# Kernel tuning notes

Measured on AMD Instinct MI355X. Metric: run time of the kernel, lower is better.

## Reference

```python
import jax, jax.numpy as jnp
import numpy as np

CAP_FACTOR = 0.125  # capacity_factor from init_kwargs


def setup_inputs() -> dict:
    key = jax.random.key(0)
    k1, k2, k3, k4 = jax.random.split(key, 4)
    B, S, D, F = 4, 4096, 1024, 4096
    x = jax.random.normal(k1, (B, S, D), jnp.float32)
    w_router = jax.random.normal(k2, (D,), jnp.float32) * (D ** -0.5)
    W1 = jax.random.normal(k3, (D, F), jnp.float32) * (D ** -0.5)
    W2 = jax.random.normal(k4, (F, D), jnp.float32) * (F ** -0.5)
    return {"x": x, "w_router": w_router, "W1": W1, "W2": W2}


def reference(x, w_router, W1, W2):
    B, S, D = x.shape
    capacity = int(S * CAP_FACTOR)  # training-mode capacity (static)

    # router: Linear(dim,1,bias=False) + sigmoid -> [B, S]
    rw = jax.nn.sigmoid(jnp.einsum('bsd,d->bs', x, w_router))

    # topk over seq dim, then sort selected indices
    _, top_idx = jax.lax.top_k(rw, capacity)          # [B, cap]
    idx_sorted = jnp.sort(top_idx, axis=1)            # router_top_indices
    order = jnp.argsort(top_idx, axis=1)              # router_top_order (in [0, cap))

    # faithful to the original code: weights gathered from router_weights at
    # `order` positions (which index the first `capacity` sequence slots)
    w_top = jnp.take_along_axis(rw, order, axis=1)    # [B, cap]

    # gather selected tokens and run the submodule (gelu MLP)
    mod_x = jnp.take_along_axis(x, idx_sorted[:, :, None], axis=1)  # [B, cap, D]
    h = jax.nn.gelu(jnp.einsum('bcd,df->bcf', mod_x, W1))
    mod_out = jnp.einsum('bcf,fd->bcd', h, W2) * w_top[:, :, None]

    # scatter back to full sequence (indices are unique per batch)
    bidx = jnp.arange(B)[:, None]
    out = jnp.zeros_like(x).at[bidx, idx_sorted].set(mod_out)

    # BCE aux loss: targets are 1 at selected positions (log clamped at -100,
    # matching F.binary_cross_entropy)
    tgt = jnp.zeros_like(rw).at[bidx, idx_sorted].set(1.0)
    logw = jnp.maximum(jnp.log(rw), -100.0)
    log1mw = jnp.maximum(jnp.log1p(-rw), -100.0)
    mod_loss = -jnp.mean(tgt * logw + (1.0 - tgt) * log1mw)

    return out, mod_loss
```

## Files before the change

kernel.cpp:

```cpp
#include <hip/hip_runtime.h>
#include <stdint.h>

#define BB 4
#define SS 4096
#define DD 1024
#define FF 4096
#define CAP 512
#define MTOT (BB*CAP)
#define NOUT (BB*SS*DD)

typedef unsigned short ushort_t;
typedef float  float4v  __attribute__((ext_vector_type(4)));
typedef short  short8v  __attribute__((ext_vector_type(8)));
typedef unsigned short ushort4v __attribute__((ext_vector_type(4)));

#define OFF_RW   0u
#define OFF_IDX  (64u*1024u)
#define OFF_WTOP (72u*1024u)
#define OFF_LOSS (80u*1024u)
#define OFF_POS  (128u*1024u)
#define OFF_RANK (256u*1024u)
#define OFF_A    (1u<<20)
#define OFF_W1T  (5u<<20)
#define OFF_W2T  (13u<<20)
#define OFF_H    (21u<<20)
#define OFF_O    (37u<<20)

#define GLD16(gsrc, ldst) __builtin_amdgcn_global_load_lds( \
    (const __attribute__((address_space(1))) void*)(gsrc),  \
    (__attribute__((address_space(3))) void*)(ldst), 16, 0, 0)

__device__ inline ushort_t f2bf(float f) {
  uint32_t u = __builtin_bit_cast(uint32_t, f);
  u = u + 0x7fffu + ((u >> 16) & 1u);
  return (ushort_t)(u >> 16);
}

__global__ void router_kernel(const float* __restrict__ x, const float* __restrict__ w,
                              float* __restrict__ rw) {
  int wave = threadIdx.x >> 6;
  int lane = threadIdx.x & 63;
  int row  = blockIdx.x * 4 + wave;
  const float4* xr = (const float4*)(x + (size_t)row * DD);
  const float4* wr = (const float4*)w;
  float s = 0.f;
#pragma unroll
  for (int i = 0; i < 4; i++) {
    float4 a = xr[lane + i * 64];
    float4 b = wr[lane + i * 64];
    s += a.x * b.x + a.y * b.y + a.z * b.z + a.w * b.w;
  }
#pragma unroll
  for (int off = 32; off > 0; off >>= 1) s += __shfl_xor(s, off, 64);
  if (lane == 0) rw[row] = 1.f / (1.f + expf(-s));
}

__global__ __launch_bounds__(256) void rank_kernel(const float* __restrict__ rw,
                                                   int* __restrict__ rank) {
  __shared__ float v[SS];
  const int b = blockIdx.y;
  const float* rwg = rw + (size_t)b * SS;
  for (int m = threadIdx.x; m < SS / 4; m += 256)
    ((float4*)v)[m] = ((const float4*)rwg)[m];
  __syncthreads();
  const int e = blockIdx.x * 64 + (threadIdx.x >> 2);
  const int part = threadIdx.x & 3;
  const float vi = v[e];
  const int j0 = part * (SS / 4);
  int cnt = 0;
#pragma unroll 4
  for (int j4 = 0; j4 < SS / 16; ++j4) {
    float4 w = ((const float4*)(v + j0))[j4];
    int j = j0 + j4 * 4;
    cnt += (w.x > vi || (w.x == vi && (j + 0) < e));
    cnt += (w.y > vi || (w.y == vi && (j + 1) < e));
    cnt += (w.z > vi || (w.z == vi && (j + 2) < e));
    cnt += (w.w > vi || (w.w == vi && (j + 3) < e));
  }
  cnt += __shfl_xor(cnt, 1, 64);
  cnt += __shfl_xor(cnt, 2, 64);
  if (part == 0) rank[(size_t)b * SS + e] = cnt;
}

__global__ __launch_bounds__(1024) void finalize_kernel(const float* __restrict__ rw,
                                                        const int* __restrict__ rank,
                                                        int* __restrict__ idxs,
                                                        float* __restrict__ wtop,
                                                        int* __restrict__ posmap,
                                                        float* __restrict__ lossP) {
  __shared__ int   wsumI[16];
  __shared__ float wsumF[16];
  const int b = blockIdx.x, tid = threadIdx.x;
  const int lane = tid & 63, wv = tid >> 6;
  const float* rwg = rw + (size_t)b * SS;
  const int*   rkg = rank + (size_t)b * SS;
  const int m0 = tid * 4;
  int rk[4]; float rv[4];
  int cnt = 0;
#pragma unroll
  for (int u = 0; u < 4; u++) {
    rk[u] = rkg[m0 + u]; rv[u] = rwg[m0 + u];
    cnt += (rk[u] < CAP);
  }
  int val = cnt;
#pragma unroll
  for (int off = 1; off < 64; off <<= 1) {
    int n = __shfl_up(val, off, 64);
    if (lane >= off) val += n;
  }
  if (lane == 63) wsumI[wv] = val;
  __syncthreads();
  int wbase = 0;
  for (int w = 0; w < wv; ++w) wbase += wsumI[w];
  int excl = wbase + val - cnt;
#pragma unroll
  for (int u = 0; u < 4; u++) {
    int m = m0 + u;
    if (rk[u] < CAP) {
      int pos = excl++;
      idxs[b * CAP + pos] = m;
      wtop[b * CAP + pos] = rwg[rk[u]];
      posmap[(size_t)b * SS + m] = b * CAP + pos;
    } else {
      posmap[(size_t)b * SS + m] = -1;
    }
  }
  float ls = 0.f;
#pragma unroll
  for (int u = 0; u < 4; u++) {
    float term = (rk[u] < CAP) ? logf(rv[u]) : log1pf(-rv[u]);
    ls += fmaxf(term, -100.f);
  }
#pragma unroll
  for (int off = 32; off > 0; off >>= 1) ls += __shfl_xor(ls, off, 64);
  if (lane == 0) wsumF[wv] = ls;
  __syncthreads();
  if (tid == 0) {
    float t = 0.f;
    for (int i = 0; i < 16; i++) t += wsumF[i];
    lossP[b] = t;
  }
}

__global__ void transpose2_kernel(const float* __restrict__ W1, ushort_t* __restrict__ W1T,
                                  const float* __restrict__ W2, ushort_t* __restrict__ W2T) {
  __shared__ float t[32][33];
  int id = blockIdx.x;
  const float* in; ushort_t* out; int R, C, bx, by;
  if (id < (FF / 32) * (DD / 32)) {
    in = W1; out = W1T; R = DD; C = FF;
    bx = id % (FF / 32); by = id / (FF / 32);
  } else {
    id -= (FF / 32) * (DD / 32);
    in = W2; out = W2T; R = FF; C = DD;
    bx = id % (DD / 32); by = id / (DD / 32);
  }
  const int c0 = bx * 32, r0 = by * 32;
  const int tx = threadIdx.x;
  const int ty = threadIdx.y;
  const float4 vv = *(const float4*)&in[(size_t)(r0 + ty) * C + c0 + tx * 4];
  t[ty][tx * 4 + 0] = vv.x; t[ty][tx * 4 + 1] = vv.y;
  t[ty][tx * 4 + 2] = vv.z; t[ty][tx * 4 + 3] = vv.w;
  __syncthreads();
  ushort4v o;
  o[0] = f2bf(t[tx * 4 + 0][ty]); o[1] = f2bf(t[tx * 4 + 1][ty]);
  o[2] = f2bf(t[tx * 4 + 2][ty]); o[3] = f2bf(t[tx * 4 + 3][ty]);
  *(ushort4v*)&out[(size_t)(c0 + ty) * R + r0 + tx * 4] = o;
}

__global__ void gather_kernel(const float* __restrict__ x, const int* __restrict__ idxs,
                              ushort_t* __restrict__ A) {
  int row = blockIdx.x;
  int b = row >> 9;
  int seq = idxs[row];
  const float4* src = (const float4*)(x + ((size_t)(b * SS + seq)) * DD);
  float4 a = src[threadIdx.x];
  ushort4v o;
  o[0] = f2bf(a.x); o[1] = f2bf(a.y); o[2] = f2bf(a.z); o[3] = f2bf(a.w);
  *(ushort4v*)(A + (size_t)row * DD + threadIdx.x * 4) = o;
}

__global__ void scatter_kernel(const float* __restrict__ O, const int* __restrict__ posmap,
                               const float* __restrict__ wtop, const float* __restrict__ lossP,
                               float* __restrict__ out) {
  int r = blockIdx.x;
  int p = posmap[r];
  float4 v = {0.f, 0.f, 0.f, 0.f};
  if (p >= 0) {
    float wt = wtop[p];
    float4 v0 = ((const float4*)(O + (size_t)p * DD))[threadIdx.x];
    float4 v1 = ((const float4*)(O + (size_t)(MTOT * DD) + (size_t)p * DD))[threadIdx.x];
    v.x = (v0.x + v1.x) * wt; v.y = (v0.y + v1.y) * wt;
    v.z = (v0.z + v1.z) * wt; v.w = (v0.w + v1.w) * wt;
  }
  ((float4*)(out + (size_t)r * DD))[threadIdx.x] = v;
  if (r == 0 && threadIdx.x == 0)
    out[NOUT] = -(lossP[0] + lossP[1] + lossP[2] + lossP[3]) / (float)(BB * SS);
}

template <int MODE>
__global__ __launch_bounds__(256) void gemm_oc(const ushort_t* __restrict__ Ag,
                                               const ushort_t* __restrict__ Bg, int Kstride,
                                               ushort_t* __restrict__ Hout,
                                               float* __restrict__ Oacc) {
  __shared__ ushort_t lA[64 * 64];
  __shared__ ushort_t lB[64 * 64];
  const int tid = threadIdx.x;
  const int lane = tid & 63, wv = tid >> 6;
  const int wr = wv >> 1, wc = wv & 1;

  const int gx = gridDim.x, gy = gridDim.y;
  const int nwg = gx * gy * gridDim.z;
  int id = blockIdx.x + gx * (blockIdx.y + gy * blockIdx.z);
  int sw = (id & 7) * (nwg >> 3) + (id >> 3);
  const int bx = sw % gx;
  const int by = (sw / gx) % gy;
  const int bz = sw / (gx * gy);

  const int bm0 = by * 64, bn0 = bx * 64;
  const int kchunk = Kstride / gridDim.z;
  const int kbeg = bz * kchunk;
  const int nkt = kchunk / 64;

  const int srow = lane >> 3;
  const int gslot = (lane & 7) ^ srow;

  float4v acc[2][2];
#pragma unroll
  for (int i = 0; i < 2; i++)
#pragma unroll
    for (int j = 0; j < 2; j++) acc[i][j] = (float4v){0.f, 0.f, 0.f, 0.f};

  for (int t = 0; t < nkt; ++t) {
    const int k0 = kbeg + t * 64;
    __syncthreads();
#pragma unroll
    for (int i = 0; i < 2; i++) {
      const int chunkbase = i * 256 + wv * 64;
      const int row = i * 32 + wv * 8 + srow;
      const ushort_t* ga = Ag + (size_t)(bm0 + row) * Kstride + k0 + gslot * 8;
      GLD16(ga, &lA[chunkbase * 8]);
    }
#pragma unroll
    for (int i = 0; i < 2; i++) {
      const int chunkbase = i * 256 + wv * 64;
      const int row = i * 32 + wv * 8 + srow;
      const ushort_t* gb = Bg + (size_t)(bn0 + row) * Kstride + k0 + gslot * 8;
      GLD16(gb, &lB[chunkbase * 8]);
    }
    __syncthreads();
#pragma unroll
    for (int kk = 0; kk < 2; kk++) {
      const int s = (lane >> 4) + kk * 4;
      short8v af[2], bfr[2];
#pragma unroll
      for (int mi = 0; mi < 2; mi++) {
        const int rr = wr * 32 + mi * 16 + (lane & 15);
        af[mi] = *(const short8v*)&lA[rr * 64 + (s ^ (rr & 7)) * 8];
      }
#pragma unroll
      for (int nj = 0; nj < 2; nj++) {
        const int rr = wc * 32 + nj * 16 + (lane & 15);
        bfr[nj] = *(const short8v*)&lB[rr * 64 + (s ^ (rr & 7)) * 8];
      }
#pragma unroll
      for (int mi = 0; mi < 2; mi++)
#pragma unroll
        for (int nj = 0; nj < 2; nj++)
          acc[mi][nj] = __builtin_amdgcn_mfma_f32_16x16x32_bf16(af[mi], bfr[nj], acc[mi][nj], 0, 0, 0);
    }
  }

  if (MODE == 0) {
#pragma unroll
    for (int mi = 0; mi < 2; mi++) {
      int r0 = bm0 + wr * 32 + mi * 16 + ((lane >> 4) << 2);
#pragma unroll
      for (int nj = 0; nj < 2; nj++) {
        int cc = bn0 + wc * 32 + nj * 16 + (lane & 15);
#pragma unroll
        for (int r = 0; r < 4; r++) {
          float xv = acc[mi][nj][r];
          float g = 0.5f * xv * (1.f + tanhf(0.7978845608028654f * (xv + 0.044715f * xv * xv * xv)));
          Hout[(size_t)(r0 + r) * FF + cc] = f2bf(g);
        }
      }
    }
  } else {
    float* Op = Oacc + (size_t)bz * MTOT * DD;
#pragma unroll
    for (int mi = 0; mi < 2; mi++) {
      int tr0 = bm0 + wr * 32 + mi * 16 + ((lane >> 4) << 2);
#pragma unroll
      for (int r = 0; r < 4; r++) {
        float* orow = Op + (size_t)(tr0 + r) * DD + bn0 + wc * 32 + (lane & 15);
#pragma unroll
        for (int nj = 0; nj < 2; nj++) orow[nj * 16] = acc[mi][nj][r];
      }
    }
  }
}

extern "C" void kernel_launch(void* const* d_in, const int* in_sizes, int n_in,
                              void* d_out, int out_size, void* d_ws, size_t ws_size,
                              hipStream_t stream) {
  (void)in_sizes; (void)n_in; (void)out_size; (void)ws_size;
  const float* x  = (const float*)d_in[0];
  const float* wrt = (const float*)d_in[1];
  const float* W1 = (const float*)d_in[2];
  const float* W2 = (const float*)d_in[3];
  float* out = (float*)d_out;
  char* ws = (char*)d_ws;
  float*    rw   = (float*)(ws + OFF_RW);
  int*      idxs = (int*)(ws + OFF_IDX);
  float*    wtop = (float*)(ws + OFF_WTOP);
  float*    lossP= (float*)(ws + OFF_LOSS);
  int*      posm = (int*)(ws + OFF_POS);
  int*      rnk  = (int*)(ws + OFF_RANK);
  ushort_t* A    = (ushort_t*)(ws + OFF_A);
  ushort_t* W1T  = (ushort_t*)(ws + OFF_W1T);
  ushort_t* W2T  = (ushort_t*)(ws + OFF_W2T);
  ushort_t* H    = (ushort_t*)(ws + OFF_H);
  float*    O    = (float*)(ws + OFF_O);

  router_kernel<<<dim3(BB * SS / 4), dim3(256), 0, stream>>>(x, wrt, rw);
  rank_kernel<<<dim3(SS / 64, BB), dim3(256), 0, stream>>>(rw, rnk);
  finalize_kernel<<<dim3(BB), dim3(1024), 0, stream>>>(rw, rnk, idxs, wtop, posm, lossP);
  transpose2_kernel<<<dim3((FF / 32) * (DD / 32) * 2), dim3(8, 32), 0, stream>>>(W1, W1T, W2, W2T);
  gather_kernel<<<dim3(MTOT), dim3(256), 0, stream>>>(x, idxs, A);
  gemm_oc<0><<<dim3(FF / 64, MTOT / 64, 1), dim3(256), 0, stream>>>(A, W1T, DD, H, nullptr);
  gemm_oc<1><<<dim3(DD / 64, MTOT / 64, 2), dim3(256), 0, stream>>>(H, W2T, FF, nullptr, O);
  scatter_kernel<<<dim3(BB * SS), dim3(256), 0, stream>>>(O, posm, wtop, lossP, out);
}
```

Measured before the change: 136.0 us.

## Deepen GEMM K-step, use XCD-aware tile mapping, split-K 4 and faster GELU

The GEMM kernel now stages two 64-wide K slices per barrier pair, a 128-deep K step that halves the number of __syncthreads per tile. Block-to-tile mapping is now chosen explicitly per XCD so neighbouring tiles share A/B rows in the same L2. The second GEMM uses split-K of 4 instead of 2, and the scatter kernel sums four partial buffers. GELU's tanh is replaced by an equivalent exp-based sigmoid form. The trade-off is twice the shared memory per block, and the larger split-K adds partial-buffer traffic that could reduce occupancy or add memory pressure.

After: 130.0 us. -4.4%, faster.

```diff
diff --git a/kernel.cpp b/kernel.cpp
--- a/kernel.cpp
+++ b/kernel.cpp
@@ -188,10 +188,15 @@
   float4 v = {0.f, 0.f, 0.f, 0.f};
   if (p >= 0) {
     float wt = wtop[p];
+    const size_t stride = (size_t)MTOT * DD;
     float4 v0 = ((const float4*)(O + (size_t)p * DD))[threadIdx.x];
-    float4 v1 = ((const float4*)(O + (size_t)(MTOT * DD) + (size_t)p * DD))[threadIdx.x];
-    v.x = (v0.x + v1.x) * wt; v.y = (v0.y + v1.y) * wt;
-    v.z = (v0.z + v1.z) * wt; v.w = (v0.w + v1.w) * wt;
+    float4 v1 = ((const float4*)(O + stride + (size_t)p * DD))[threadIdx.x];
+    float4 v2 = ((const float4*)(O + 2 * stride + (size_t)p * DD))[threadIdx.x];
+    float4 v3 = ((const float4*)(O + 3 * stride + (size_t)p * DD))[threadIdx.x];
+    v.x = ((v0.x + v1.x) + (v2.x + v3.x)) * wt;
+    v.y = ((v0.y + v1.y) + (v2.y + v3.y)) * wt;
+    v.z = ((v0.z + v1.z) + (v2.z + v3.z)) * wt;
+    v.w = ((v0.w + v1.w) + (v2.w + v3.w)) * wt;
   }
   ((float4*)(out + (size_t)r * DD))[threadIdx.x] = v;
   if (r == 0 && threadIdx.x == 0)
@@ -203,24 +208,29 @@
                                                const ushort_t* __restrict__ Bg, int Kstride,
                                                ushort_t* __restrict__ Hout,
                                                float* __restrict__ Oacc) {
-  __shared__ ushort_t lA[64 * 64];
-  __shared__ ushort_t lB[64 * 64];
+  __shared__ ushort_t lA[2][64 * 64];
+  __shared__ ushort_t lB[2][64 * 64];
   const int tid = threadIdx.x;
   const int lane = tid & 63, wv = tid >> 6;
   const int wr = wv >> 1, wc = wv & 1;
 
   const int gx = gridDim.x, gy = gridDim.y;
-  const int nwg = gx * gy * gridDim.z;
-  int id = blockIdx.x + gx * (blockIdx.y + gy * blockIdx.z);
-  int sw = (id & 7) * (nwg >> 3) + (id >> 3);
-  const int bx = sw % gx;
-  const int by = (sw / gx) % gy;
-  const int bz = sw / (gx * gy);
-
-  const int bm0 = by * 64, bn0 = bx * 64;
-  const int kchunk = Kstride / gridDim.z;
-  const int kbeg = bz * kchunk;
-  const int nkt = kchunk / 64;
+  const int id = blockIdx.x + gx * (blockIdx.y + gy * blockIdx.z);
+  const int xcd = id & 7, q = id >> 3;
+
+  int bm0, bn0, bz, kbeg;
+  if (MODE == 0) {
+    const int mx = (xcd & 1) * 16 + (q & 15);
+    const int nx = (xcd >> 1) * 16 + (q >> 4);
+    bm0 = mx * 64; bn0 = nx * 64; bz = 0; kbeg = 0;
+  } else {
+    bz = xcd >> 1;
+    const int by = (xcd & 1) * 16 + (q & 15);
+    const int bx = q >> 4;
+    bm0 = by * 64; bn0 = bx * 64; kbeg = bz * (Kstride >> 2);
+  }
+  const int kchunk = (MODE == 0) ? Kstride : (Kstride >> 2);
+  const int nkt = kchunk / 128;
 
   const int srow = lane >> 3;
   const int gslot = (lane & 7) ^ srow;
@@ -232,36 +242,33 @@
     for (int j = 0; j < 2; j++) acc[i][j] = (float4v){0.f, 0.f, 0.f, 0.f};
 
   for (int t = 0; t < nkt; ++t) {
-    const int k0 = kbeg + t * 64;
+    const int k0 = kbeg + t * 128;
     __syncthreads();
 #pragma unroll
-    for (int i = 0; i < 2; i++) {
-      const int chunkbase = i * 256 + wv * 64;
-      const int row = i * 32 + wv * 8 + srow;
-      const ushort_t* ga = Ag + (size_t)(bm0 + row) * Kstride + k0 + gslot * 8;
-      GLD16(ga, &lA[chunkbase * 8]);
-    }
-#pragma unroll
-    for (int i = 0; i < 2; i++) {
-      const int chunkbase = i * 256 + wv * 64;
-      const int row = i * 32 + wv * 8 + srow;
-      const ushort_t* gb = Bg + (size_t)(bn0 + row) * Kstride + k0 + gslot * 8;
-      GLD16(gb, &lB[chunkbase * 8]);
+    for (int p = 0; p < 2; p++) {
+#pragma unroll
+      for (int i = 0; i < 2; i++) {
+        const int row = i * 32 + wv * 8 + srow;
+        const int chunkbase = i * 256 + wv * 64;
+        GLD16(Ag + (size_t)(bm0 + row) * Kstride + k0 + p * 64 + gslot * 8, &lA[p][chunkbase * 8]);
+        GLD16(Bg + (size_t)(bn0 + row) * Kstride + k0 + p * 64 + gslot * 8, &lB[p][chunkbase * 8]);
+      }
     }
     __syncthreads();
 #pragma unroll
-    for (int kk = 0; kk < 2; kk++) {
-      const int s = (lane >> 4) + kk * 4;
+    for (int kk = 0; kk < 4; kk++) {
+      const int pl = kk >> 1;
+      const int s = (lane >> 4) + (kk & 1) * 4;
       short8v af[2], bfr[2];
 #pragma unroll
       for (int mi = 0; mi < 2; mi++) {
         const int rr = wr * 32 + mi * 16 + (lane & 15);
-        af[mi] = *(const short8v*)&lA[rr * 64 + (s ^ (rr & 7)) * 8];
+        af[mi] = *(const short8v*)&lA[pl][rr * 64 + (s ^ (rr & 7)) * 8];
       }
 #pragma unroll
       for (int nj = 0; nj < 2; nj++) {
         const int rr = wc * 32 + nj * 16 + (lane & 15);
-        bfr[nj] = *(const short8v*)&lB[rr * 64 + (s ^ (rr & 7)) * 8];
+        bfr[nj] = *(const short8v*)&lB[pl][rr * 64 + (s ^ (rr & 7)) * 8];
       }
 #pragma unroll
       for (int mi = 0; mi < 2; mi++)
@@ -281,7 +288,8 @@
 #pragma unroll
         for (int r = 0; r < 4; r++) {
           float xv = acc[mi][nj][r];
-          float g = 0.5f * xv * (1.f + tanhf(0.7978845608028654f * (xv + 0.044715f * xv * xv * xv)));
+          float u = 0.7978845608028654f * (xv + 0.044715f * xv * xv * xv);
+          float g = xv / (1.f + __expf(-2.f * u));
           Hout[(size_t)(r0 + r) * FF + cc] = f2bf(g);
         }
       }
@@ -329,6 +337,6 @@
   transpose2_kernel<<<dim3((FF / 32) * (DD / 32) * 2), dim3(8, 32), 0, stream>>>(W1, W1T, W2, W2T);
   gather_kernel<<<dim3(MTOT), dim3(256), 0, stream>>>(x, idxs, A);
   gemm_oc<0><<<dim3(FF / 64, MTOT / 64, 1), dim3(256), 0, stream>>>(A, W1T, DD, H, nullptr);
-  gemm_oc<1><<<dim3(DD / 64, MTOT / 64, 2), dim3(256), 0, stream>>>(H, W2T, FF, nullptr, O);
+  gemm_oc<1><<<dim3(DD / 64, MTOT / 64, 4), dim3(256), 0, stream>>>(H, W2T, FF, nullptr, O);
   scatter_kernel<<<dim3(BB * SS), dim3(256), 0, stream>>>(O, posm, wtop, lossP, out);
 }
```
